# Kernel optimization log

Hardware: AMD Instinct MI355X
Metric: run time of the kernel (lower is better)

## Reference

```python
import jax, jax.numpy as jnp
import numpy as np

VOCAB, EMBED, HIDDEN, NUM_CLASSES, PAD_IDX = 50257, 128, 128, 4, 0
B, T = 256, 512


def setup_inputs() -> dict:
    key = jax.random.key(0)
    ks = jax.random.split(key, 10)
    x = jax.random.randint(ks[0], (B, T), 0, VOCAB)
    h0 = jnp.zeros((B, HIDDEN), dtype=jnp.float32)
    # embedding: uniform(-0.1, 0.1), pad row zeroed (matches init_weights)
    emb = jax.random.uniform(ks[1], (VOCAB, EMBED), jnp.float32, -0.1, 0.1)
    emb = emb.at[PAD_IDX].set(0.0)
    def xavier(k, shape):
        fan_out, fan_in = shape
        bound = float(np.sqrt(6.0 / (fan_in + fan_out)))
        return jax.random.uniform(k, shape, jnp.float32, -bound, bound)
    W_ih = xavier(ks[2], (HIDDEN, EMBED))      # rnn.weight_ih_l0
    W_hh = xavier(ks[3], (HIDDEN, HIDDEN))     # rnn.weight_hh_l0
    b_ih = jnp.zeros((HIDDEN,), jnp.float32)
    b_hh = jnp.zeros((HIDDEN,), jnp.float32)
    W1 = xavier(ks[4], (2 * HIDDEN, HIDDEN))   # output_layer1
    b1 = jnp.zeros((2 * HIDDEN,), jnp.float32)
    W2 = xavier(ks[5], (NUM_CLASSES, 2 * HIDDEN))  # output_layer2
    b2 = jnp.zeros((NUM_CLASSES,), jnp.float32)
    return {"x": x, "h0": h0, "emb": emb, "W_ih": W_ih, "W_hh": W_hh,
            "b_ih": b_ih, "b_hh": b_hh, "W1": W1, "b1": b1, "W2": W2, "b2": b2}


def reference(x, h0, emb, W_ih, W_hh, b_ih, b_hh, W1, b1, W2, b2):
    # Embedding lookup (dropout layers are identity in eval mode)
    embedded = emb[x]                                    # [B, T, E]
    # Precompute input projection for every step, then scan the recurrence.
    x_proj = jnp.einsum('bte,he->bth', embedded, W_ih) + b_ih + b_hh  # [B, T, H]
    x_proj_t = jnp.swapaxes(x_proj, 0, 1)                # [T, B, H]

    def step(h, xp):
        h_new = jnp.tanh(xp + h @ W_hh.T)                # [B, H]
        return h_new, None

    last_hidden, _ = jax.lax.scan(step, h0, x_proj_t)    # [B, H]
    # MLP head: Linear -> ReLU -> Linear
    hidden_mlp = jax.nn.relu(last_hidden @ W1.T + b1)    # [B, 2H]
    logits = hidden_mlp @ W2.T + b2                      # [B, C]
    return (logits, last_hidden)
```

## Files before the change

kernel.cpp:

```cpp
#include <hip/hip_runtime.h>
#include <hip/hip_bf16.h>
#include <math.h>

#define BB 256
#define TT 512
#define EE 128
#define HH 128
#define NC 4
#define MM (BB * TT)

typedef __bf16 bf16x8 __attribute__((ext_vector_type(8)));
typedef __bf16 bf16x4 __attribute__((ext_vector_type(4)));
typedef float  f32x4  __attribute__((ext_vector_type(4)));

__device__ __forceinline__ float fast_tanh(float x) {
    float t = __builtin_amdgcn_exp2f(x * 2.885390081777927f);
    return 1.f - 2.f * __builtin_amdgcn_rcpf(1.f + t);
}

template <typename XPT>
__global__ __launch_bounds__(256, 3) void embed_gemm(
    const int* __restrict__ x, const float* __restrict__ emb,
    const float* __restrict__ Wih, const float* __restrict__ bih,
    const float* __restrict__ bhh, XPT* __restrict__ xpout)
{
    const int tid = threadIdx.x;
    const int m0  = blockIdx.x * 64;

    const int LDW = 72;
    const int LDE = 132;
    __shared__ __align__(16) char smem[36864 + 512];
    __bf16* Wh     = (__bf16*)smem;
    __bf16* Wl     = (__bf16*)(smem + 18432);
    float*  epi    = (float*)smem;
    float*  bias_s = (float*)(smem + 36864);

    if (tid < 128) bias_s[tid] = bih[tid] + bhh[tid];

    const int lane = tid & 63, wid = tid >> 6;
    const int col  = lane & 15, quad = lane >> 4;

    const int gi = x[m0 + wid * 16 + col];
    const float* arow = emb + (size_t)gi * 128;

    f32x4 acc[8];
#pragma unroll
    for (int nt = 0; nt < 8; ++nt) acc[nt] = f32x4{0.f, 0.f, 0.f, 0.f};

#pragma unroll
    for (int half = 0; half < 2; ++half) {
#pragma unroll
        for (int it = 0; it < 8; ++it) {
            int c   = it * 256 + tid;
            int row = c >> 4;
            int seg = c & 15;
            float4 wv = ((const float4*)Wih)[row * 32 + half * 16 + seg];
            bf16x4 wh, wl;
            wh[0] = (__bf16)wv.x; wl[0] = (__bf16)(wv.x - (float)wh[0]);
            wh[1] = (__bf16)wv.y; wl[1] = (__bf16)(wv.y - (float)wh[1]);
            wh[2] = (__bf16)wv.z; wl[2] = (__bf16)(wv.z - (float)wh[2]);
            wh[3] = (__bf16)wv.w; wl[3] = (__bf16)(wv.w - (float)wh[3]);
            *(bf16x4*)&Wh[row * LDW + seg * 4] = wh;
            *(bf16x4*)&Wl[row * LDW + seg * 4] = wl;
        }
        __syncthreads();

#pragma unroll
        for (int kk = 0; kk < 2; ++kk) {
            const float* ap = arow + half * 64 + kk * 32 + quad * 8;
            f32x4 a0 = *(const f32x4*)ap;
            f32x4 a1 = *(const f32x4*)(ap + 4);
            bf16x8 afh, afl;
#pragma unroll
            for (int u = 0; u < 4; ++u) {
                afh[u]     = (__bf16)a0[u]; afl[u]     = (__bf16)(a0[u] - (float)afh[u]);
                afh[u + 4] = (__bf16)a1[u]; afl[u + 4] = (__bf16)(a1[u] - (float)afh[u + 4]);
            }
#pragma unroll
            for (int nt = 0; nt < 8; ++nt) {
                int ro = (nt * 16 + col) * LDW + kk * 32 + quad * 8;
                bf16x8 wfh = *(const bf16x8*)&Wh[ro];
                bf16x8 wfl = *(const bf16x8*)&Wl[ro];
                acc[nt] = __builtin_amdgcn_mfma_f32_16x16x32_bf16(afh, wfh, acc[nt], 0, 0, 0);
                acc[nt] = __builtin_amdgcn_mfma_f32_16x16x32_bf16(afl, wfh, acc[nt], 0, 0, 0);
                acc[nt] = __builtin_amdgcn_mfma_f32_16x16x32_bf16(afh, wfl, acc[nt], 0, 0, 0);
            }
        }
        __syncthreads();
    }

#pragma unroll
    for (int nt = 0; nt < 8; ++nt) {
        int n = nt * 16 + col;
        float bs = bias_s[n];
#pragma unroll
        for (int r = 0; r < 4; ++r)
            epi[(wid * 16 + quad * 4 + r) * LDE + n] = acc[nt][r] + bs;
    }
    __syncthreads();

#pragma unroll
    for (int it = 0; it < 8; ++it) {
        int c   = it * 256 + tid;
        int row = c >> 5;
        int cf  = c & 31;
        f32x4 v = *(const f32x4*)&epi[row * LDE + cf * 4];
        if (sizeof(XPT) == 4) {
            *(f32x4*)&((float*)xpout)[(size_t)(m0 + row) * 128 + cf * 4] = v;
        } else {
            bf16x4 bv;
            bv[0] = (__bf16)v[0]; bv[1] = (__bf16)v[1];
            bv[2] = (__bf16)v[2]; bv[3] = (__bf16)v[3];
            *(bf16x4*)&((__bf16*)xpout)[(size_t)(m0 + row) * 128 + cf * 4] = bv;
        }
    }
}

template <typename XPT>
__global__ __launch_bounds__(256, 1) void rnn_scan(
    const XPT* __restrict__ xp, const float* __restrict__ Whh,
    const float* __restrict__ h0, float* __restrict__ hlast)
{
    const int b    = blockIdx.x;
    const int tid  = threadIdx.x;
    const int q    = tid >> 6;
    const int lane = tid & 63;

    __shared__ float h_s[128];
    __shared__ float part[4 * 128];

    f32x4 wA[8], wB[8];
    {
        const float* r0 = Whh + (size_t)lane * 128 + q * 32;
        const float* r1 = Whh + (size_t)(lane + 64) * 128 + q * 32;
#pragma unroll
        for (int c = 0; c < 8; ++c) {
            wA[c] = *(const f32x4*)(r0 + c * 4);
            wB[c] = *(const f32x4*)(r1 + c * 4);
        }
    }
#pragma unroll
    for (int c = 0; c < 8; ++c)
        asm volatile("" : "+v"(wA[c]), "+v"(wB[c]));

    if (tid < 128) h_s[tid] = h0[b * 128 + tid];

    const XPT* xpb = xp + (size_t)b * (TT * 128);
    float xv[8];
#pragma unroll
    for (int s = 0; s < 8; ++s)
        xv[s] = (tid < 128) ? (float)xpb[s * 128 + tid] : 0.f;
    __syncthreads();

    for (int tw = 0; tw < TT; tw += 8) {
#pragma unroll
        for (int ts = 0; ts < 8; ++ts) {
            const float* hq = &h_s[q * 32];
            f32x4 h4[8];
#pragma unroll
            for (int u = 0; u < 8; ++u) h4[u] = *(const f32x4*)&hq[u * 4];

            f32x4 aA = f32x4{0.f, 0.f, 0.f, 0.f};
            f32x4 aB = f32x4{0.f, 0.f, 0.f, 0.f};
#pragma unroll
            for (int u = 0; u < 8; ++u) {
                aA += wA[u] * h4[u];
                aB += wB[u] * h4[u];
            }
            part[q * 128 + lane]      = (aA[0] + aA[1]) + (aA[2] + aA[3]);
            part[q * 128 + 64 + lane] = (aB[0] + aB[1]) + (aB[2] + aB[3]);
            __syncthreads();
            if (tid < 128) {
                float s = (part[tid] + part[128 + tid])
                        + (part[256 + tid] + part[384 + tid]);
                h_s[tid] = fast_tanh(s + xv[ts]);
                if (tw + 8 < TT)
                    xv[ts] = (float)xpb[(size_t)(tw + 8 + ts) * 128 + tid];
            }
            __syncthreads();
        }
    }
    if (tid < 128) hlast[b * 128 + tid] = h_s[tid];
}

__global__ __launch_bounds__(256, 2) void mlp_head(
    const float* __restrict__ hlast, const float* __restrict__ W1,
    const float* __restrict__ b1, const float* __restrict__ W2,
    const float* __restrict__ b2, float* __restrict__ out)
{
    const int b = blockIdx.x, tid = threadIdx.x;
    __shared__ float h_row[128];
    __shared__ float hid[256];

    if (tid < 128) {
        float hv = hlast[b * 128 + tid];
        h_row[tid] = hv;
        out[1024 + b * 128 + tid] = hv;
    }
    __syncthreads();

    {
        float acc = b1[tid];
        const float4* wrow = (const float4*)(W1 + (size_t)tid * 128);
#pragma unroll
        for (int k4 = 0; k4 < 32; ++k4) {
            float4 wv = wrow[k4];
            acc += wv.x * h_row[k4 * 4 + 0] + wv.y * h_row[k4 * 4 + 1]
                 + wv.z * h_row[k4 * 4 + 2] + wv.w * h_row[k4 * 4 + 3];
        }
        hid[tid] = fmaxf(acc, 0.f);
    }
    __syncthreads();

    const int wv = tid >> 6, lane = tid & 63;
    float s = 0.f;
#pragma unroll
    for (int qq = 0; qq < 4; ++qq)
        s += hid[qq * 64 + lane] * W2[wv * 256 + qq * 64 + lane];
#pragma unroll
    for (int off = 32; off > 0; off >>= 1) s += __shfl_down(s, off);
    if (lane == 0) out[b * 4 + wv] = s + b2[wv];
}

extern "C" void kernel_launch(void* const* d_in, const int* in_sizes, int n_in,
                              void* d_out, int out_size, void* d_ws, size_t ws_size,
                              hipStream_t stream)
{
    const int*   x   = (const int*)d_in[0];
    const float* h0  = (const float*)d_in[1];
    const float* emb = (const float*)d_in[2];
    const float* Wih = (const float*)d_in[3];
    const float* Whh = (const float*)d_in[4];
    const float* bih = (const float*)d_in[5];
    const float* bhh = (const float*)d_in[6];
    const float* W1  = (const float*)d_in[7];
    const float* b1  = (const float*)d_in[8];
    const float* W2  = (const float*)d_in[9];
    const float* b2  = (const float*)d_in[10];
    float* out = (float*)d_out;

    const size_t xp_f32_bytes = (size_t)MM * 128 * sizeof(float);
    const size_t hl_bytes     = (size_t)BB * 128 * sizeof(float);

    if (ws_size >= xp_f32_bytes + hl_bytes) {
        float* xpw = (float*)d_ws;
        float* hl  = (float*)((char*)d_ws + xp_f32_bytes);
        embed_gemm<float><<<MM / 64, 256, 0, stream>>>(x, emb, Wih, bih, bhh, xpw);
        rnn_scan<float><<<BB, 256, 0, stream>>>(xpw, Whh, h0, hl);
        mlp_head<<<BB, 256, 0, stream>>>(hl, W1, b1, W2, b2, out);
    } else {
        __bf16* xpw = (__bf16*)d_ws;
        float*  hl  = (float*)((char*)d_ws + (size_t)MM * 128 * sizeof(__bf16));
        embed_gemm<__bf16><<<MM / 64, 256, 0, stream>>>(x, emb, Wih, bih, bhh, xpw);
        rnn_scan<__bf16><<<BB, 256, 0, stream>>>(xpw, Whh, h0, hl);
        mlp_head<<<BB, 256, 0, stream>>>(hl, W1, b1, W2, b2, out);
    }
}
```

Before: 276.8 us.

## Halve per-step barriers in RNN scan via wave-owned hidden slices; fuse MLP head

Each wave now owns the 32 hidden entries it consumes. After a single barrier per timestep, the wave's own lanes finalize those entries, so the second barrier per step is gone. The partial-sum buffer is double-buffered so the next step's writes cannot race with reads, and a raw waitcnt+s_barrier replaces __syncthreads. The MLP head is fused into the scan kernel, which removes a launch and the hidden-state round trip through global memory. The risk is that correctness relies on in-wave ordering of LDS accesses.

```diff
diff --git a/kernel.cpp b/kernel.cpp
--- a/kernel.cpp
+++ b/kernel.cpp
@@ -16,6 +16,10 @@
 __device__ __forceinline__ float fast_tanh(float x) {
     float t = __builtin_amdgcn_exp2f(x * 2.885390081777927f);
     return 1.f - 2.f * __builtin_amdgcn_rcpf(1.f + t);
+}
+
+__device__ __forceinline__ void bar_lds() {
+    asm volatile("s_waitcnt lgkmcnt(0)\n\ts_barrier" ::: "memory");
 }
 
 template <typename XPT>
@@ -117,17 +121,24 @@
 }
 
 template <typename XPT>
-__global__ __launch_bounds__(256, 1) void rnn_scan(
+__global__ __launch_bounds__(256, 1) void rnn_scan_mlp(
     const XPT* __restrict__ xp, const float* __restrict__ Whh,
-    const float* __restrict__ h0, float* __restrict__ hlast)
+    const float* __restrict__ h0, const float* __restrict__ W1,
+    const float* __restrict__ b1, const float* __restrict__ W2,
+    const float* __restrict__ b2, float* __restrict__ out)
 {
     const int b    = blockIdx.x;
     const int tid  = threadIdx.x;
     const int q    = tid >> 6;
     const int lane = tid & 63;
-
-    __shared__ float h_s[128];
-    __shared__ float part[4 * 128];
+    const int l32  = lane & 31;
+    const bool owner = (lane < 32);
+    const int o = q * 32 + l32;
+
+    __shared__ float h_priv[4][32];
+    __shared__ float part[2][4][128];
+    __shared__ float h_full[128];
+    __shared__ float hid[256];
 
     f32x4 wA[8], wB[8];
     {
@@ -143,61 +154,49 @@
     for (int c = 0; c < 8; ++c)
         asm volatile("" : "+v"(wA[c]), "+v"(wB[c]));
 
-    if (tid < 128) h_s[tid] = h0[b * 128 + tid];
+    if (owner) h_priv[q][l32] = h0[b * 128 + o];
 
     const XPT* xpb = xp + (size_t)b * (TT * 128);
     float xv[8];
 #pragma unroll
     for (int s = 0; s < 8; ++s)
-        xv[s] = (tid < 128) ? (float)xpb[s * 128 + tid] : 0.f;
-    __syncthreads();
-
-    for (int tw = 0; tw < TT; tw += 8) {
-#pragma unroll
-        for (int ts = 0; ts < 8; ++ts) {
-            const float* hq = &h_s[q * 32];
-            f32x4 h4[8];
-#pragma unroll
-            for (int u = 0; u < 8; ++u) h4[u] = *(const f32x4*)&hq[u * 4];
-
-            f32x4 aA = f32x4{0.f, 0.f, 0.f, 0.f};
-            f32x4 aB = f32x4{0.f, 0.f, 0.f, 0.f};
-#pragma unroll
-            for (int u = 0; u < 8; ++u) {
-                aA += wA[u] * h4[u];
-                aB += wB[u] * h4[u];
-            }
-            part[q * 128 + lane]      = (aA[0] + aA[1]) + (aA[2] + aA[3]);
-            part[q * 128 + 64 + lane] = (aB[0] + aB[1]) + (aB[2] + aB[3]);
-            __syncthreads();
-            if (tid < 128) {
-                float s = (part[tid] + part[128 + tid])
-                        + (part[256 + tid] + part[384 + tid]);
-                h_s[tid] = fast_tanh(s + xv[ts]);
-                if (tw + 8 < TT)
-                    xv[ts] = (float)xpb[(size_t)(tw + 8 + ts) * 128 + tid];
-            }
-            __syncthreads();
-        }
-    }
-    if (tid < 128) hlast[b * 128 + tid] = h_s[tid];
-}
-
-__global__ __launch_bounds__(256, 2) void mlp_head(
-    const float* __restrict__ hlast, const float* __restrict__ W1,
-    const float* __restrict__ b1, const float* __restrict__ W2,
-    const float* __restrict__ b2, float* __restrict__ out)
-{
-    const int b = blockIdx.x, tid = threadIdx.x;
-    __shared__ float h_row[128];
-    __shared__ float hid[256];
-
-    if (tid < 128) {
-        float hv = hlast[b * 128 + tid];
-        h_row[tid] = hv;
-        out[1024 + b * 128 + tid] = hv;
-    }
-    __syncthreads();
+        xv[s] = owner ? (float)xpb[s * 128 + o] : 0.f;
+
+    bar_lds();
+
+    for (int t = 0; t < TT; ++t) {
+        const int p = t & 1;
+        const float* hq = &h_priv[q][0];
+        f32x4 h4[8];
+#pragma unroll
+        for (int u = 0; u < 8; ++u) h4[u] = *(const f32x4*)&hq[u * 4];
+
+        f32x4 aA = f32x4{0.f, 0.f, 0.f, 0.f};
+        f32x4 aB = f32x4{0.f, 0.f, 0.f, 0.f};
+#pragma unroll
+        for (int u = 0; u < 8; ++u) {
+            aA += wA[u] * h4[u];
+            aB += wB[u] * h4[u];
+        }
+        part[p][q][lane]      = (aA[0] + aA[1]) + (aA[2] + aA[3]);
+        part[p][q][64 + lane] = (aB[0] + aB[1]) + (aB[2] + aB[3]);
+
+        bar_lds();
+
+        if (owner) {
+            float s = (part[p][0][o] + part[p][1][o])
+                    + (part[p][2][o] + part[p][3][o]);
+            float hv = fast_tanh(s + xv[t & 7]);
+            h_priv[q][l32] = hv;
+            if (t + 8 < TT)
+                xv[t & 7] = (float)xpb[(size_t)(t + 8) * 128 + o];
+        }
+    }
+
+    if (owner) h_full[o] = h_priv[q][l32];
+    bar_lds();
+
+    if (tid < 128) out[1024 + b * 128 + tid] = h_full[tid];
 
     {
         float acc = b1[tid];
@@ -205,21 +204,20 @@
 #pragma unroll
         for (int k4 = 0; k4 < 32; ++k4) {
             float4 wv = wrow[k4];
-            acc += wv.x * h_row[k4 * 4 + 0] + wv.y * h_row[k4 * 4 + 1]
-                 + wv.z * h_row[k4 * 4 + 2] + wv.w * h_row[k4 * 4 + 3];
+            acc += wv.x * h_full[k4 * 4 + 0] + wv.y * h_full[k4 * 4 + 1]
+                 + wv.z * h_full[k4 * 4 + 2] + wv.w * h_full[k4 * 4 + 3];
         }
         hid[tid] = fmaxf(acc, 0.f);
     }
     __syncthreads();
 
-    const int wv = tid >> 6, lane = tid & 63;
     float s = 0.f;
 #pragma unroll
     for (int qq = 0; qq < 4; ++qq)
-        s += hid[qq * 64 + lane] * W2[wv * 256 + qq * 64 + lane];
+        s += hid[qq * 64 + lane] * W2[q * 256 + qq * 64 + lane];
 #pragma unroll
     for (int off = 32; off > 0; off >>= 1) s += __shfl_down(s, off);
-    if (lane == 0) out[b * 4 + wv] = s + b2[wv];
+    if (lane == 0) out[b * 4 + q] = s + b2[q];
 }
 
 extern "C" void kernel_launch(void* const* d_in, const int* in_sizes, int n_in,
@@ -240,19 +238,14 @@
     float* out = (float*)d_out;
 
     const size_t xp_f32_bytes = (size_t)MM * 128 * sizeof(float);
-    const size_t hl_bytes     = (size_t)BB * 128 * sizeof(float);
-
-    if (ws_size >= xp_f32_bytes + hl_bytes) {
+
+    if (ws_size >= xp_f32_bytes) {
         float* xpw = (float*)d_ws;
-        float* hl  = (float*)((char*)d_ws + xp_f32_bytes);
         embed_gemm<float><<<MM / 64, 256, 0, stream>>>(x, emb, Wih, bih, bhh, xpw);
-        rnn_scan<float><<<BB, 256, 0, stream>>>(xpw, Whh, h0, hl);
-        mlp_head<<<BB, 256, 0, stream>>>(hl, W1, b1, W2, b2, out);
+        rnn_scan_mlp<float><<<BB, 256, 0, stream>>>(xpw, Whh, h0, W1, b1, W2, b2, out);
     } else {
         __bf16* xpw = (__bf16*)d_ws;
-        float*  hl  = (float*)((char*)d_ws + (size_t)MM * 128 * sizeof(__bf16));
         embed_gemm<__bf16><<<MM / 64, 256, 0, stream>>>(x, emb, Wih, bih, bhh, xpw);
-        rnn_scan<__bf16><<<BB, 256, 0, stream>>>(xpw, Whh, h0, hl);
-        mlp_head<<<BB, 256, 0, stream>>>(hl, W1, b1, W2, b2, out);
-    }
-}
+        rnn_scan_mlp<__bf16><<<BB, 256, 0, stream>>>(xpw, Whh, h0, W1, b1, W2, b2, out);
+    }
+}
```

Measured after the change: 443.1 us. 60.1% more time.
